# Optimization experiments

Measured on AMD Instinct MI355X. Metric: run time of the kernel, lower is better.

## Reference

```python
import jax, jax.numpy as jnp
import numpy as np
from jax import lax

# Poincare ball, curvature c = 1.0 (geoopt default for CustomPoincare)
SQRT_C = 1.0
BALL_EPS = 1e-3   # projx margin (geoopt-style)
MIN_NORM = 1e-7
BN_EPS = 1e-5


def _norm(x):
    # norm over channel (last) dim, clamped away from 0
    return jnp.maximum(jnp.linalg.norm(x, axis=-1, keepdims=True), MIN_NORM)


def projx(x):
    # clip points back inside the ball of radius (1-eps)/sqrt(c)
    maxnorm = (1.0 - BALL_EPS) / SQRT_C
    n = _norm(x)
    return x * jnp.minimum(1.0, maxnorm / n)


def expmap0(v):
    # exp map at the origin: tanh(sqrt(c)||v||) * v / (sqrt(c)||v||)
    n = _norm(v)
    return projx(jnp.tanh(SQRT_C * n) * v / (SQRT_C * n))


def logmap0(x):
    # log map at the origin: artanh(sqrt(c)||x||) * x / (sqrt(c)||x||)
    n = _norm(x)
    t = jnp.minimum(SQRT_C * n, 1.0 - 1e-5)
    return jnp.arctanh(t) * x / (SQRT_C * n)


def setup_inputs() -> dict:
    key = jax.random.key(0)
    k0, k1 = jax.random.split(key)
    B, C_in, H, W, C_out = 16, 3, 224, 224, 64
    x = jax.random.normal(k0, (B, C_in, H, W), dtype=jnp.float32)
    # Kaiming-ish init for the 3x3 stem conv, HWIO layout
    fan_in = 3 * 3 * C_in
    conv_w = jax.random.normal(k1, (3, 3, C_in, C_out), dtype=jnp.float32) * np.float32(np.sqrt(2.0 / fan_in))
    conv_b = jnp.zeros((C_out,), dtype=jnp.float32)
    bn_gamma = jnp.ones((C_out,), dtype=jnp.float32)
    bn_beta = jnp.zeros((C_out,), dtype=jnp.float32)
    return {"x": x, "conv_w": conv_w, "conv_b": conv_b,
            "bn_gamma": bn_gamma, "bn_beta": bn_beta}


def reference(x, conv_w, conv_b, bn_gamma, bn_beta):
    # x: [B, C, H, W] -> NHWC (channel-last points on the Poincare ball)
    h = jnp.transpose(x, (0, 2, 3, 1))
    h = projx(h)

    # --- PoincareConv2d: tangent-space 3x3 conv (log0 -> conv+bias -> exp0) ---
    u = logmap0(h)
    u = lax.conv_general_dilated(
        u, conv_w, window_strides=(1, 1), padding="SAME",
        dimension_numbers=("NHWC", "HWIO", "NHWC"))
    u = u + conv_b
    h = expmap0(u)

    # --- PoincareBatchNorm2d: tangent-space BN over (B,H,W) per channel ---
    u = logmap0(h)
    mean = jnp.mean(u, axis=(0, 1, 2), keepdims=True)
    var = jnp.var(u, axis=(0, 1, 2), keepdims=True)
    u = (u - mean) * lax.rsqrt(var + BN_EPS) * bn_gamma + bn_beta
    h = expmap0(u)

    # --- PoincareTangentReLU ---
    h = expmap0(jax.nn.relu(logmap0(h)))
    return h  # [B, H, W, C_out]
```

## Files before the change

kernel.cpp:

```cpp
#include <hip/hip_runtime.h>
#include <math.h>

#define B_ 16
#define H_ 224
#define W_ 224
#define HP_ 226
#define WP_ 226
#define CIN_ 3
#define COUT_ 64
#define NPIX_ (B_ * H_ * W_)
#define NPAD_ (B_ * HP_ * WP_)
#define NBLK_ (NPIX_ / 256)
#define MAXNORM_ 0.999f
#define MINN_ 1e-7f
#define TCL_ (1.0f - 1e-5f)
#define LCLAMP_ 3.8002012f
#define BN_EPS_ 1e-5f
#define NF_ ((float)NPIX_)
#define PADW2_ 36

typedef float v4f __attribute__((ext_vector_type(4)));

struct Acc8 {
  v4f v0, v1, v2, v3, v4, v5, v6, v7;
};

#define EACH8(X) X(0) X(1) X(2) X(3) X(4) X(5) X(6) X(7)

__global__ void k0_transform(const float* __restrict__ x, float4* __restrict__ u0p) {
  int idx = blockIdx.x * 256 + threadIdx.x;
  if (idx >= NPAD_) return;
  int b = idx / (HP_ * WP_);
  int r = idx % (HP_ * WP_);
  int yp = r / WP_, xp = r % WP_;
  float4 o = make_float4(0.f, 0.f, 0.f, 0.f);
  if (yp >= 1 && yp <= H_ && xp >= 1 && xp <= W_) {
    const float* xb = x + (size_t)b * (CIN_ * H_ * W_) + (size_t)(yp - 1) * W_ + (xp - 1);
    float v0 = xb[0];
    float v1 = xb[H_ * W_];
    float v2 = xb[2 * H_ * W_];
    float n = sqrtf(fmaf(v0, v0, fmaf(v1, v1, v2 * v2)));
    float ncl = fmaxf(n, MINN_);
    float s = fminf(1.0f, MAXNORM_ / ncl);
    float p0 = v0 * s, p1 = v1 * s, p2 = v2 * s;
    float np_ = fmaxf(sqrtf(fmaf(p0, p0, fmaf(p1, p1, p2 * p2))), MINN_);
    float t = fminf(np_, TCL_);
    float ath = 0.5f * __logf(__fdividef(1.0f + t, 1.0f - t));
    float f = __fdividef(ath, np_);
    o.x = p0 * f; o.y = p1 * f; o.z = p2 * f;
  }
  u0p[idx] = o;
}

__device__ __forceinline__ void conv_half(const float4* __restrict__ u0p,
                                          const float* __restrict__ wgt,
                                          const float* __restrict__ bias,
                                          int pix, int h, Acc8& a) {
  int b = pix / (H_ * W_);
  int r = pix % (H_ * W_);
  int y = r / W_, x = r % W_;
  const float4* base = u0p + ((size_t)b * HP_ + y) * WP_ + x;
  const v4f* b4 = (const v4f*)bias;
  int h8 = h * 8;
#define INIT(i) a.v##i = b4[h8 + i];
  EACH8(INIT)
#undef INIT
#define FMA_X(i) a.v##i += in.x * wp[h8 + i];
#define FMA_Y(i) a.v##i += in.y * wp[16 + h8 + i];
#define FMA_Z(i) a.v##i += in.z * wp[32 + h8 + i];
#define TAP(t) { float4 in = base[((t) / 3) * WP_ + ((t) % 3)];              \
                 const v4f* wp = (const v4f*)(wgt + (t) * 3 * COUT_);        \
                 EACH8(FMA_X) EACH8(FMA_Y) EACH8(FMA_Z) }
  TAP(0) TAP(1) TAP(2) TAP(3) TAP(4) TAP(5) TAP(6) TAP(7) TAP(8)
#undef TAP
#undef FMA_X
#undef FMA_Y
#undef FMA_Z
}

__device__ __forceinline__ v4f vshfl_xor(v4f v, int m) {
  v4f r;
  r.x = __shfl_xor(v.x, m, 64);
  r.y = __shfl_xor(v.y, m, 64);
  r.z = __shfl_xor(v.z, m, 64);
  r.w = __shfl_xor(v.w, m, 64);
  return r;
}
__device__ __forceinline__ v4f vrelu(v4f v) {
  v.x = fmaxf(v.x, 0.f); v.y = fmaxf(v.y, 0.f);
  v.z = fmaxf(v.z, 0.f); v.w = fmaxf(v.w, 0.f);
  return v;
}
__device__ __forceinline__ float hsum(v4f v) { return (v.x + v.y) + (v.z + v.w); }

__global__ void __launch_bounds__(256, 4)
k1_stats(const float4* __restrict__ u0p, const float* __restrict__ wgt,
         const float* __restrict__ bias, float* __restrict__ partials) {
  int pix = blockIdx.x * 256 + threadIdx.x;
  __shared__ __align__(16) float stg[4 * 64 * PADW2_];
  __shared__ float scl[256];
  __shared__ float red_s[256], red_q[256];
  int lane = threadIdx.x & 63, wid = threadIdx.x >> 6;
  float* row = stg + (size_t)(wid * 64 + lane) * PADW2_;
  int pr8 = lane >> 3, qi = lane & 7;
  const float* rb = stg + (size_t)wid * 64 * PADW2_ + pr8 * PADW2_ + qi * 4;
  const float* scrow = scl + wid * 64;

  Acc8 a;
  conv_half(u0p, wgt, bias, pix, 0, a);
  v4f s2v = (v4f)0.0f;
#define SQ(i) s2v += a.v##i * a.v##i;
  EACH8(SQ)
#undef SQ
  float s2A = hsum(s2v);
#define STG(i) *(v4f*)(row + 4 * (i)) = a.v##i;
  EACH8(STG)
#undef STG
  __builtin_amdgcn_wave_barrier();

  conv_half(u0p, wgt, bias, pix, 1, a);
  s2v = (v4f)0.0f;
#define SQ(i) s2v += a.v##i * a.v##i;
  EACH8(SQ)
#undef SQ
  float n2 = s2A + hsum(s2v);
  float n = sqrtf(n2);
  float sc = (n > LCLAMP_) ? (LCLAMP_ / n) : 1.0f;
  scl[wid * 64 + lane] = sc;
  __builtin_amdgcn_wave_barrier();

  v4f sA = (v4f)0.0f, qA = (v4f)0.0f;
#pragma unroll
  for (int j = 0; j < 8; j++) {
    float g = scrow[j * 8 + pr8];
    v4f v = *(const v4f*)(rb + j * 8 * PADW2_) * g;
    sA += v; qA += v * v;
  }
  sA += vshfl_xor(sA, 8);  qA += vshfl_xor(qA, 8);
  sA += vshfl_xor(sA, 16); qA += vshfl_xor(qA, 16);
  sA += vshfl_xor(sA, 32); qA += vshfl_xor(qA, 32);
  if (lane < 8) {
    *(v4f*)&red_s[wid * 32 + qi * 4] = sA;
    *(v4f*)&red_q[wid * 32 + qi * 4] = qA;
  }
  __builtin_amdgcn_wave_barrier();

#define STG(i) *(v4f*)(row + 4 * (i)) = a.v##i;
  EACH8(STG)
#undef STG
  __builtin_amdgcn_wave_barrier();
  v4f sB = (v4f)0.0f, qB = (v4f)0.0f;
#pragma unroll
  for (int j = 0; j < 8; j++) {
    float g = scrow[j * 8 + pr8];
    v4f v = *(const v4f*)(rb + j * 8 * PADW2_) * g;
    sB += v; qB += v * v;
  }
  sB += vshfl_xor(sB, 8);  qB += vshfl_xor(qB, 8);
  sB += vshfl_xor(sB, 16); qB += vshfl_xor(qB, 16);
  sB += vshfl_xor(sB, 32); qB += vshfl_xor(qB, 32);
  if (lane < 8) {
    *(v4f*)&red_s[128 + wid * 32 + qi * 4] = sB;
    *(v4f*)&red_q[128 + wid * 32 + qi * 4] = qB;
  }
  __syncthreads();
  int tid = threadIdx.x;
  if (tid < 128) {
    int c = tid & 63;
    int base = (c >> 5) * 128 + (c & 31);
    const float* rr = (tid < 64) ? red_s : red_q;
    float tot = rr[base] + rr[base + 32] + rr[base + 64] + rr[base + 96];
    partials[(size_t)blockIdx.x * 128 + tid] = tot;
  }
}

__global__ void k2_finalize(const float* __restrict__ partials, const float* __restrict__ gamma,
                            float* __restrict__ stats) {
  int c = blockIdx.x;
  int t = threadIdx.x;
  float s = 0.f, q = 0.f;
  for (int i = t; i < NBLK_; i += 256) {
    s += partials[(size_t)i * 128 + c];
    q += partials[(size_t)i * 128 + 64 + c];
  }
  __shared__ float ls[256], lq[256];
  ls[t] = s; lq[t] = q;
  __syncthreads();
#pragma unroll
  for (int off = 128; off > 0; off >>= 1) {
    if (t < off) { ls[t] += ls[t + off]; lq[t] += lq[t + off]; }
    __syncthreads();
  }
  if (t == 0) {
    float mean = ls[0] / NF_;
    float msq  = lq[0] / NF_;
    float var = msq - mean * mean;
    stats[c] = mean;
    stats[64 + c] = gamma[c] / sqrtf(var + BN_EPS_);
  }
}

__global__ void __launch_bounds__(256, 4)
k3_final(const float4* __restrict__ u0p, const float* __restrict__ wgt,
         const float* __restrict__ bias, const float* __restrict__ stats,
         const float* __restrict__ beta, float* __restrict__ out) {
  int pix = blockIdx.x * 256 + threadIdx.x;
  __shared__ __align__(16) float stg[4 * 64 * PADW2_];
  __shared__ float gl[256];
  int lane = threadIdx.x & 63, wid = threadIdx.x >> 6;
  float* row = stg + (size_t)(wid * 64 + lane) * PADW2_;
  int pr8 = lane >> 3, qi = lane & 7;
  const float* rb = stg + (size_t)wid * 64 * PADW2_ + pr8 * PADW2_ + qi * 4;
  const float* grow = gl + wid * 64;
  v4f* outw = (v4f*)out + ((size_t)blockIdx.x * 256 + wid * 64) * 16;

  const v4f* mean4 = (const v4f*)stats;
  const v4f* rg4   = (const v4f*)(stats + 64);
  const v4f* beta4 = (const v4f*)beta;

  Acc8 a;
  conv_half(u0p, wgt, bias, pix, 0, a);
  v4f s2v = (v4f)0.0f, r2v = (v4f)0.0f;
#define BNA(i) { a.v##i = (a.v##i - mean4[i]) * rg4[i] + beta4[i];           \
                 s2v += a.v##i * a.v##i; v4f t_ = vrelu(a.v##i); r2v += t_ * t_; }
  EACH8(BNA)
#undef BNA
  float nv2 = hsum(s2v), r2 = hsum(r2v);
#define STG(i) *(v4f*)(row + 4 * (i)) = a.v##i;
  EACH8(STG)
#undef STG
  __builtin_amdgcn_wave_barrier();

  conv_half(u0p, wgt, bias, pix, 1, a);
  s2v = (v4f)0.0f; r2v = (v4f)0.0f;
#define BNB(i) { a.v##i = (a.v##i - mean4[8 + i]) * rg4[8 + i] + beta4[8 + i]; \
                 s2v += a.v##i * a.v##i; v4f t_ = vrelu(a.v##i); r2v += t_ * t_; }
  EACH8(BNB)
#undef BNB
  nv2 += hsum(s2v); r2 += hsum(r2v);
  float nv = sqrtf(nv2);
  float sv = (nv > LCLAMP_) ? (LCLAMP_ / nv) : 1.0f;
  float nw = fmaxf(sv * sqrtf(r2), MINN_);
  float e2 = __expf(2.0f * nw);
  float th = 1.0f - __fdividef(2.0f, e2 + 1.0f);
  float se = __fdividef(th, nw);
  float clip = fminf(1.0f, MAXNORM_ / fmaxf(th, MINN_));
  float g = se * clip * sv;
  gl[wid * 64 + lane] = g;
  __builtin_amdgcn_wave_barrier();

#pragma unroll
  for (int j = 0; j < 8; j++) {
    float gv = grow[j * 8 + pr8];
    v4f v = vrelu(*(const v4f*)(rb + j * 8 * PADW2_)) * gv;
    __builtin_nontemporal_store(v, outw + (j * 8 + pr8) * 16 + qi);
  }
  __builtin_amdgcn_wave_barrier();

#define STG(i) *(v4f*)(row + 4 * (i)) = a.v##i;
  EACH8(STG)
#undef STG
  __builtin_amdgcn_wave_barrier();
#pragma unroll
  for (int j = 0; j < 8; j++) {
    float gv = grow[j * 8 + pr8];
    v4f v = vrelu(*(const v4f*)(rb + j * 8 * PADW2_)) * gv;
    __builtin_nontemporal_store(v, outw + (j * 8 + pr8) * 16 + 8 + qi);
  }
}

extern "C" void kernel_launch(void* const* d_in, const int* in_sizes, int n_in,
                              void* d_out, int out_size, void* d_ws, size_t ws_size,
                              hipStream_t stream) {
  const float* x     = (const float*)d_in[0];
  const float* wgt   = (const float*)d_in[1];
  const float* bias  = (const float*)d_in[2];
  const float* gamma = (const float*)d_in[3];
  const float* beta  = (const float*)d_in[4];
  float* out = (float*)d_out;

  char* ws = (char*)d_ws;
  float4* u0p      = (float4*)ws;
  float*  partials = (float*)(ws + (size_t)NPAD_ * 16);
  float*  stats    = (float*)(ws + (size_t)NPAD_ * 16 + (size_t)NBLK_ * 128 * 4);

  hipLaunchKernelGGL(k0_transform, dim3((NPAD_ + 255) / 256), dim3(256), 0, stream, x, u0p);
  hipLaunchKernelGGL(k1_stats,     dim3(NBLK_),               dim3(256), 0, stream, u0p, wgt, bias, partials);
  hipLaunchKernelGGL(k2_finalize,  dim3(64),                  dim3(256), 0, stream, partials, gamma, stats);
  hipLaunchKernelGGL(k3_final,     dim3(NBLK_),               dim3(256), 0, stream, u0p, wgt, bias, stats, beta, out);
}
```

Before: 311.1 us.

## Compute two pixels per thread and stage conv weights in LDS

Each thread now computes the 3x3 conv for two pixels at once, so every weight vector read is reused for two accumulator sets, and each block covers 512 pixels. Conv weights, bias and the BN parameters are copied into shared memory at block start instead of being read from global/scalar memory. The goal is to halve weight-load traffic per FMA and cut the number of blocks. In exchange, register pressure doubles (launch bounds lowered from 4 to 3 waves) and LDS usage grows.

```diff
diff --git a/kernel.cpp b/kernel.cpp
--- a/kernel.cpp
+++ b/kernel.cpp
@@ -10,7 +10,7 @@
 #define COUT_ 64
 #define NPIX_ (B_ * H_ * W_)
 #define NPAD_ (B_ * HP_ * WP_)
-#define NBLK_ (NPIX_ / 256)
+#define NBLK2_ (NPIX_ / 512)
 #define MAXNORM_ 0.999f
 #define MINN_ 1e-7f
 #define TCL_ (1.0f - 1e-5f)
@@ -21,10 +21,7 @@
 
 typedef float v4f __attribute__((ext_vector_type(4)));
 
-struct Acc8 {
-  v4f v0, v1, v2, v3, v4, v5, v6, v7;
-};
-
+struct Acc8 { v4f v0, v1, v2, v3, v4, v5, v6, v7; };
 #define EACH8(X) X(0) X(1) X(2) X(3) X(4) X(5) X(6) X(7)
 
 __global__ void k0_transform(const float* __restrict__ x, float4* __restrict__ u0p) {
@@ -52,30 +49,32 @@
   u0p[idx] = o;
 }
 
-__device__ __forceinline__ void conv_half(const float4* __restrict__ u0p,
-                                          const float* __restrict__ wgt,
-                                          const float* __restrict__ bias,
-                                          int pix, int h, Acc8& a) {
-  int b = pix / (H_ * W_);
-  int r = pix % (H_ * W_);
-  int y = r / W_, x = r % W_;
-  const float4* base = u0p + ((size_t)b * HP_ + y) * WP_ + x;
-  const v4f* b4 = (const v4f*)bias;
+__device__ __forceinline__ void conv_pair_half(
+    const float4* __restrict__ u0p, const v4f* __restrict__ wq,
+    const v4f* __restrict__ bq, int px0, int px1, int h,
+    Acc8& a0, Acc8& a1) {
+  int b0 = px0 / (H_ * W_), r0 = px0 % (H_ * W_);
+  int y0 = r0 / W_, x0 = r0 % W_;
+  int b1 = px1 / (H_ * W_), r1 = px1 % (H_ * W_);
+  int y1 = r1 / W_, x1 = r1 % W_;
+  const float4* base0 = u0p + ((size_t)b0 * HP_ + y0) * WP_ + x0;
+  const float4* base1 = u0p + ((size_t)b1 * HP_ + y1) * WP_ + x1;
   int h8 = h * 8;
-#define INIT(i) a.v##i = b4[h8 + i];
+#define INIT(i) { v4f bv = bq[h8 + i]; a0.v##i = bv; a1.v##i = bv; }
   EACH8(INIT)
 #undef INIT
-#define FMA_X(i) a.v##i += in.x * wp[h8 + i];
-#define FMA_Y(i) a.v##i += in.y * wp[16 + h8 + i];
-#define FMA_Z(i) a.v##i += in.z * wp[32 + h8 + i];
-#define TAP(t) { float4 in = base[((t) / 3) * WP_ + ((t) % 3)];              \
-                 const v4f* wp = (const v4f*)(wgt + (t) * 3 * COUT_);        \
-                 EACH8(FMA_X) EACH8(FMA_Y) EACH8(FMA_Z) }
+#define FX(i) { v4f w = wp[i];      a0.v##i += in0.x * w; a1.v##i += in1.x * w; }
+#define FY(i) { v4f w = wp[16 + i]; a0.v##i += in0.y * w; a1.v##i += in1.y * w; }
+#define FZ(i) { v4f w = wp[32 + i]; a0.v##i += in0.z * w; a1.v##i += in1.z * w; }
+#define TAP(t) { float4 in0 = base0[((t) / 3) * WP_ + ((t) % 3)];            \
+                 float4 in1 = base1[((t) / 3) * WP_ + ((t) % 3)];            \
+                 const v4f* wp = wq + (t) * 48 + h8;                         \
+                 EACH8(FX) EACH8(FY) EACH8(FZ) }
   TAP(0) TAP(1) TAP(2) TAP(3) TAP(4) TAP(5) TAP(6) TAP(7) TAP(8)
 #undef TAP
-#undef FMA_X
-#undef FMA_Y
-#undef FMA_Z
+#undef FX
+#undef FY
+#undef FZ
 }
 
 __device__ __forceinline__ v4f vshfl_xor(v4f v, int m) {
@@ -93,78 +92,96 @@
 }
 __device__ __forceinline__ float hsum(v4f v) { return (v.x + v.y) + (v.z + v.w); }
 
-__global__ void __launch_bounds__(256, 4)
+#define STAGE8(acc) do {                                                     \
+  *(v4f*)(row + 0)  = acc.v0; *(v4f*)(row + 4)  = acc.v1;                    \
+  *(v4f*)(row + 8)  = acc.v2; *(v4f*)(row + 12) = acc.v3;                    \
+  *(v4f*)(row + 16) = acc.v4; *(v4f*)(row + 20) = acc.v5;                    \
+  *(v4f*)(row + 24) = acc.v6; *(v4f*)(row + 28) = acc.v7;                    \
+} while (0)
+
+__global__ void __launch_bounds__(256, 3)
 k1_stats(const float4* __restrict__ u0p, const float* __restrict__ wgt,
          const float* __restrict__ bias, float* __restrict__ partials) {
-  int pix = blockIdx.x * 256 + threadIdx.x;
   __shared__ __align__(16) float stg[4 * 64 * PADW2_];
-  __shared__ float scl[256];
+  __shared__ __align__(16) v4f wlds[432];
+  __shared__ __align__(16) v4f blds[16];
+  __shared__ float scl[512];
   __shared__ float red_s[256], red_q[256];
-  int lane = threadIdx.x & 63, wid = threadIdx.x >> 6;
+  int tid = threadIdx.x;
+  {
+    const v4f* wg = (const v4f*)wgt;
+    wlds[tid] = wg[tid];
+    if (tid < 176) wlds[256 + tid] = wg[256 + tid];
+    if (tid < 16) blds[tid] = ((const v4f*)bias)[tid];
+  }
+  __syncthreads();
+
+  int px0 = blockIdx.x * 512 + tid;
+  int px1 = px0 + 256;
+  int lane = tid & 63, wid = tid >> 6;
   float* row = stg + (size_t)(wid * 64 + lane) * PADW2_;
   int pr8 = lane >> 3, qi = lane & 7;
   const float* rb = stg + (size_t)wid * 64 * PADW2_ + pr8 * PADW2_ + qi * 4;
-  const float* scrow = scl + wid * 64;
-
-  Acc8 a;
-  conv_half(u0p, wgt, bias, pix, 0, a);
-  v4f s2v = (v4f)0.0f;
-#define SQ(i) s2v += a.v##i * a.v##i;
-  EACH8(SQ)
-#undef SQ
-  float s2A = hsum(s2v);
-#define STG(i) *(v4f*)(row + 4 * (i)) = a.v##i;
-  EACH8(STG)
-#undef STG
-  __builtin_amdgcn_wave_barrier();
-
-  conv_half(u0p, wgt, bias, pix, 1, a);
-  s2v = (v4f)0.0f;
-#define SQ(i) s2v += a.v##i * a.v##i;
-  EACH8(SQ)
-#undef SQ
-  float n2 = s2A + hsum(s2v);
-  float n = sqrtf(n2);
-  float sc = (n > LCLAMP_) ? (LCLAMP_ / n) : 1.0f;
-  scl[wid * 64 + lane] = sc;
-  __builtin_amdgcn_wave_barrier();
-
-  v4f sA = (v4f)0.0f, qA = (v4f)0.0f;
-#pragma unroll
-  for (int j = 0; j < 8; j++) {
-    float g = scrow[j * 8 + pr8];
-    v4f v = *(const v4f*)(rb + j * 8 * PADW2_) * g;
-    sA += v; qA += v * v;
-  }
+  const float* sc_s0 = scl + wid * 64;
+  const float* sc_s1 = scl + 256 + wid * 64;
+
+  Acc8 xA0, xA1;
+  conv_pair_half(u0p, wlds, blds, px0, px1, 0, xA0, xA1);
+  v4f t0 = (v4f)0.0f, t1 = (v4f)0.0f;
+#define SQ2(i) { t0 += xA0.v##i * xA0.v##i; t1 += xA1.v##i * xA1.v##i; }
+  EACH8(SQ2)
+#undef SQ2
+  float s20 = hsum(t0), s21 = hsum(t1);
+  STAGE8(xA0);
+  __builtin_amdgcn_wave_barrier();
+
+  Acc8 xB0, xB1;
+  conv_pair_half(u0p, wlds, blds, px0, px1, 1, xB0, xB1);
+  t0 = (v4f)0.0f; t1 = (v4f)0.0f;
+#define SQ2(i) { t0 += xB0.v##i * xB0.v##i; t1 += xB1.v##i * xB1.v##i; }
+  EACH8(SQ2)
+#undef SQ2
+  s20 += hsum(t0); s21 += hsum(t1);
+  float n0 = sqrtf(s20), n1 = sqrtf(s21);
+  scl[wid * 64 + lane]       = (n0 > LCLAMP_) ? (LCLAMP_ / n0) : 1.0f;
+  scl[256 + wid * 64 + lane] = (n1 > LCLAMP_) ? (LCLAMP_ / n1) : 1.0f;
+  __builtin_amdgcn_wave_barrier();
+
+  v4f sA = (v4f)0.0f, qA = (v4f)0.0f, sB = (v4f)0.0f, qB = (v4f)0.0f;
+#define READROUND(sv, qv, scp)                                               \
+  _Pragma("unroll") for (int j = 0; j < 8; j++) {                            \
+    float g = (scp)[j * 8 + pr8];                                            \
+    v4f v = *(const v4f*)(rb + j * 8 * PADW2_) * g;                          \
+    sv += v; qv += v * v;                                                    \
+  }
+  READROUND(sA, qA, sc_s0)
+  __builtin_amdgcn_wave_barrier();
+  STAGE8(xA1);
+  __builtin_amdgcn_wave_barrier();
+  READROUND(sA, qA, sc_s1)
+  __builtin_amdgcn_wave_barrier();
+  STAGE8(xB0);
+  __builtin_amdgcn_wave_barrier();
+  READROUND(sB, qB, sc_s0)
+  __builtin_amdgcn_wave_barrier();
+  STAGE8(xB1);
+  __builtin_amdgcn_wave_barrier();
+  READROUND(sB, qB, sc_s1)
+#undef READROUND
+
   sA += vshfl_xor(sA, 8);  qA += vshfl_xor(qA, 8);
   sA += vshfl_xor(sA, 16); qA += vshfl_xor(qA, 16);
   sA += vshfl_xor(sA, 32); qA += vshfl_xor(qA, 32);
-  if (lane < 8) {
-    *(v4f*)&red_s[wid * 32 + qi * 4] = sA;
-    *(v4f*)&red_q[wid * 32 + qi * 4] = qA;
-  }
-  __builtin_amdgcn_wave_barrier();
-
-#define STG(i) *(v4f*)(row + 4 * (i)) = a.v##i;
-  EACH8(STG)
-#undef STG
-  __builtin_amdgcn_wave_barrier();
-  v4f sB = (v4f)0.0f, qB = (v4f)0.0f;
-#pragma unroll
-  for (int j = 0; j < 8; j++) {
-    float g = scrow[j * 8 + pr8];
-    v4f v = *(const v4f*)(rb + j * 8 * PADW2_) * g;
-    sB += v; qB += v * v;
-  }
   sB += vshfl_xor(sB, 8);  qB += vshfl_xor(qB, 8);
   sB += vshfl_xor(sB, 16); qB += vshfl_xor(qB, 16);
   sB += vshfl_xor(sB, 32); qB += vshfl_xor(qB, 32);
   if (lane < 8) {
+    *(v4f*)&red_s[wid * 32 + qi * 4] = sA;
+    *(v4f*)&red_q[wid * 32 + qi * 4] = qA;
     *(v4f*)&red_s[128 + wid * 32 + qi * 4] = sB;
     *(v4f*)&red_q[128 + wid * 32 + qi * 4] = qB;
   }
   __syncthreads();
-  int tid = threadIdx.x;
   if (tid < 128) {
     int c = tid & 63;
     int base = (c >> 5) * 128 + (c & 31);
@@ -179,7 +196,7 @@
   int c = blockIdx.x;
   int t = threadIdx.x;
   float s = 0.f, q = 0.f;
-  for (int i = t; i < NBLK_; i += 256) {
+  for (int i = t; i < NBLK2_; i += 256) {
     s += partials[(size_t)i * 128 + c];
     q += partials[(size_t)i * 128 + 64 + c];
   }
@@ -200,44 +217,7 @@
   }
 }
 
-__global__ void __launch_bounds__(256, 4)
-k3_final(const float4* __restrict__ u0p, const float* __restrict__ wgt,
-         const float* __restrict__ bias, const float* __restrict__ stats,
-         const float* __restrict__ beta, float* __restrict__ out) {
-  int pix = blockIdx.x * 256 + threadIdx.x;
-  __shared__ __align__(16) float stg[4 * 64 * PADW2_];
-  __shared__ float gl[256];
-  int lane = threadIdx.x & 63, wid = threadIdx.x >> 6;
-  float* row = stg + (size_t)(wid * 64 + lane) * PADW2_;
-  int pr8 = lane >> 3, qi = lane & 7;
-  const float* rb = stg + (size_t)wid * 64 * PADW2_ + pr8 * PADW2_ + qi * 4;
-  const float* grow = gl + wid * 64;
-  v4f* outw = (v4f*)out + ((size_t)blockIdx.x * 256 + wid * 64) * 16;
-
-  const v4f* mean4 = (const v4f*)stats;
-  const v4f* rg4   = (const v4f*)(stats + 64);
-  const v4f* beta4 = (const v4f*)beta;
-
-  Acc8 a;
-  conv_half(u0p, wgt, bias, pix, 0, a);
-  v4f s2v = (v4f)0.0f, r2v = (v4f)0.0f;
-#define BNA(i) { a.v##i = (a.v##i - mean4[i]) * rg4[i] + beta4[i];           \
-                 s2v += a.v##i * a.v##i; v4f t_ = vrelu(a.v##i); r2v += t_ * t_; }
-  EACH8(BNA)
-#undef BNA
-  float nv2 = hsum(s2v), r2 = hsum(r2v);
-#define STG(i) *(v4f*)(row + 4 * (i)) = a.v##i;
-  EACH8(STG)
-#undef STG
-  __builtin_amdgcn_wave_barrier();
-
-  conv_half(u0p, wgt, bias, pix, 1, a);
-  s2v = (v4f)0.0f; r2v = (v4f)0.0f;
-#define BNB(i) { a.v##i = (a.v##i - mean4[8 + i]) * rg4[8 + i] + beta4[8 + i]; \
-                 s2v += a.v##i * a.v##i; v4f t_ = vrelu(a.v##i); r2v += t_ * t_; }
-  EACH8(BNB)
-#undef BNB
-  nv2 += hsum(s2v); r2 += hsum(r2v);
+__device__ __forceinline__ float out_scale(float nv2, float r2) {
   float nv = sqrtf(nv2);
   float sv = (nv > LCLAMP_) ? (LCLAMP_ / nv) : 1.0f;
   float nw = fmaxf(sv * sqrtf(r2), MINN_);
@@ -245,28 +225,89 @@
   float th = 1.0f - __fdividef(2.0f, e2 + 1.0f);
   float se = __fdividef(th, nw);
   float clip = fminf(1.0f, MAXNORM_ / fmaxf(th, MINN_));
-  float g = se * clip * sv;
-  gl[wid * 64 + lane] = g;
-  __builtin_amdgcn_wave_barrier();
-
-#pragma unroll
-  for (int j = 0; j < 8; j++) {
-    float gv = grow[j * 8 + pr8];
-    v4f v = vrelu(*(const v4f*)(rb + j * 8 * PADW2_)) * gv;
-    __builtin_nontemporal_store(v, outw + (j * 8 + pr8) * 16 + qi);
-  }
-  __builtin_amdgcn_wave_barrier();
-
-#define STG(i) *(v4f*)(row + 4 * (i)) = a.v##i;
-  EACH8(STG)
-#undef STG
-  __builtin_amdgcn_wave_barrier();
-#pragma unroll
-  for (int j = 0; j < 8; j++) {
-    float gv = grow[j * 8 + pr8];
-    v4f v = vrelu(*(const v4f*)(rb + j * 8 * PADW2_)) * gv;
-    __builtin_nontemporal_store(v, outw + (j * 8 + pr8) * 16 + 8 + qi);
-  }
+  return se * clip * sv;
+}
+
+__global__ void __launch_bounds__(256, 3)
+k3_final(const float4* __restrict__ u0p, const float* __restrict__ wgt,
+         const float* __restrict__ bias, const float* __restrict__ stats,
+         const float* __restrict__ beta, float* __restrict__ out) {
+  __shared__ __align__(16) float stg[4 * 64 * PADW2_];
+  __shared__ __align__(16) v4f wlds[432];
+  __shared__ __align__(16) v4f blds[16];
+  __shared__ __align__(16) v4f m4[16], rg4[16], bt4[16];
+  __shared__ float gl[512];
+  int tid = threadIdx.x;
+  {
+    const v4f* wg = (const v4f*)wgt;
+    wlds[tid] = wg[tid];
+    if (tid < 176) wlds[256 + tid] = wg[256 + tid];
+    if (tid < 16) {
+      blds[tid] = ((const v4f*)bias)[tid];
+      m4[tid]   = ((const v4f*)stats)[tid];
+      rg4[tid]  = ((const v4f*)(stats + 64))[tid];
+      bt4[tid]  = ((const v4f*)beta)[tid];
+    }
+  }
+  __syncthreads();
+
+  int px0 = blockIdx.x * 512 + tid;
+  int px1 = px0 + 256;
+  int lane = tid & 63, wid = tid >> 6;
+  float* row = stg + (size_t)(wid * 64 + lane) * PADW2_;
+  int pr8 = lane >> 3, qi = lane & 7;
+  const float* rb = stg + (size_t)wid * 64 * PADW2_ + pr8 * PADW2_ + qi * 4;
+  const float* gl_s0 = gl + wid * 64;
+  const float* gl_s1 = gl + 256 + wid * 64;
+  v4f* outw0 = (v4f*)out + ((size_t)blockIdx.x * 512 + wid * 64) * 16;
+  v4f* outw1 = outw0 + (size_t)256 * 16;
+
+  Acc8 xA0, xA1;
+  conv_pair_half(u0p, wlds, blds, px0, px1, 0, xA0, xA1);
+  v4f sa0 = (v4f)0.0f, ra0 = (v4f)0.0f, sa1 = (v4f)0.0f, ra1 = (v4f)0.0f;
+#define BNA(i) {                                                             \
+    xA0.v##i = (xA0.v##i - m4[i]) * rg4[i] + bt4[i];                         \
+    sa0 += xA0.v##i * xA0.v##i; v4f r_ = vrelu(xA0.v##i); ra0 += r_ * r_;    \
+    xA1.v##i = (xA1.v##i - m4[i]) * rg4[i] + bt4[i];                         \
+    sa1 += xA1.v##i * xA1.v##i; v4f p_ = vrelu(xA1.v##i); ra1 += p_ * p_; }
+  EACH8(BNA)
+#undef BNA
+  STAGE8(xA0);
+  __builtin_amdgcn_wave_barrier();
+
+  Acc8 xB0, xB1;
+  conv_pair_half(u0p, wlds, blds, px0, px1, 1, xB0, xB1);
+#define BNB(i) {                                                             \
+    xB0.v##i = (xB0.v##i - m4[8 + i]) * rg4[8 + i] + bt4[8 + i];             \
+    sa0 += xB0.v##i * xB0.v##i; v4f r_ = vrelu(xB0.v##i); ra0 += r_ * r_;    \
+    xB1.v##i = (xB1.v##i - m4[8 + i]) * rg4[8 + i] + bt4[8 + i];             \
+    sa1 += xB1.v##i * xB1.v##i; v4f p_ = vrelu(xB1.v##i); ra1 += p_ * p_; }
+  EACH8(BNB)
+#undef BNB
+  gl[wid * 64 + lane]       = out_scale(hsum(sa0), hsum(ra0));
+  gl[256 + wid * 64 + lane] = out_scale(hsum(sa1), hsum(ra1));
+  __builtin_amdgcn_wave_barrier();
+
+#define STOREROUND(ow, gp, choff)                                            \
+  _Pragma("unroll") for (int j = 0; j < 8; j++) {                            \
+    float g = (gp)[j * 8 + pr8];                                             \
+    v4f v = vrelu(*(const v4f*)(rb + j * 8 * PADW2_)) * g;                   \
+    __builtin_nontemporal_store(v, (ow) + (size_t)(j * 8 + pr8) * 16 + (choff) + qi); \
+  }
+  STOREROUND(outw0, gl_s0, 0)
+  __builtin_amdgcn_wave_barrier();
+  STAGE8(xA1);
+  __builtin_amdgcn_wave_barrier();
+  STOREROUND(outw1, gl_s1, 0)
+  __builtin_amdgcn_wave_barrier();
+  STAGE8(xB0);
+  __builtin_amdgcn_wave_barrier();
+  STOREROUND(outw0, gl_s0, 8)
+  __builtin_amdgcn_wave_barrier();
+  STAGE8(xB1);
+  __builtin_amdgcn_wave_barrier();
+  STOREROUND(outw1, gl_s1, 8)
+#undef STOREROUND
 }
 
 extern "C" void kernel_launch(void* const* d_in, const int* in_sizes, int n_in,
@@ -282,10 +323,10 @@
   char* ws = (char*)d_ws;
   float4* u0p      = (float4*)ws;
   float*  partials = (float*)(ws + (size_t)NPAD_ * 16);
-  float*  stats    = (float*)(ws + (size_t)NPAD_ * 16 + (size_t)NBLK_ * 128 * 4);
+  float*  stats    = (float*)(ws + (size_t)NPAD_ * 16 + (size_t)NBLK2_ * 128 * 4);
 
   hipLaunchKernelGGL(k0_transform, dim3((NPAD_ + 255) / 256), dim3(256), 0, stream, x, u0p);
-  hipLaunchKernelGGL(k1_stats,     dim3(NBLK_),               dim3(256), 0, stream, u0p, wgt, bias, partials);
+  hipLaunchKernelGGL(k1_stats,     dim3(NBLK2_),              dim3(256), 0, stream, u0p, wgt, bias, partials);
   hipLaunchKernelGGL(k2_finalize,  dim3(64),                  dim3(256), 0, stream, partials, gamma, stats);
-  hipLaunchKernelGGL(k3_final,     dim3(NBLK_),               dim3(256), 0, stream, u0p, wgt, bias, stats, beta, out);
-}
+  hipLaunchKernelGGL(k3_final,     dim3(NBLK2_),              dim3(256), 0, stream, u0p, wgt, bias, stats, beta, out);
+}
```

Measured after the change: 365.9 us. +17.6%, slower.
